# Kernel tuning notes

Measured on AMD Instinct MI355X. Metric: run time of the kernel, lower is better.

The kernel has to match this reference:

```python
import jax, jax.numpy as jnp
import numpy as np

B, N, D, E, H, K = 2, 2048, 1024, 8, 2048, 2


def setup_inputs() -> dict:
    key = jax.random.key(0)
    ks = jax.random.split(key, 5)
    s = 0.02  # init scale
    return {
        "x": jax.random.normal(ks[0], (B, N, D), dtype=jnp.float32),
        "w_gate": jax.random.normal(ks[1], (D, E), dtype=jnp.float32) * s,
        "b_gate": jnp.zeros((E,), dtype=jnp.float32),
        "w1": jax.random.normal(ks[2], (E, D, H), dtype=jnp.float32) * s,
        "b1": jnp.zeros((E, H), dtype=jnp.float32),
        "w2": jax.random.normal(ks[3], (E, H, D), dtype=jnp.float32) * s,
        "b2": jnp.zeros((E, D), dtype=jnp.float32),
    }


def reference(x, w_gate, b_gate, w1, b1, w2, b2):
    b, n, d = x.shape
    T = b * n
    xf = x.reshape(T, d)                                   # (T, D)
    # --- top-k routing ---
    logits = xf @ w_gate + b_gate                          # (T, E)
    topk_logits, topk_idx = jax.lax.top_k(logits, K)       # (T, K)
    topk_gates = jax.nn.softmax(topk_logits, axis=-1)      # softmax over selected experts
    entropy = -(topk_gates * jnp.log(jnp.clip(topk_gates, 1e-8, None))).sum(-1).mean()
    # scatter top-k gates into full (T, E) gate matrix (zeros for unselected)
    gates = jnp.zeros_like(logits).at[jnp.arange(T)[:, None], topk_idx].add(topk_gates)
    # --- expert MLPs (dense over experts; gates zero out unselected) ---
    h = jax.nn.relu(jnp.einsum('td,edh->eth', xf, w1) + b1[:, None, :])  # (E, T, H)
    y = jnp.einsum('eth,ehd->etd', h, w2) + b2[:, None, :]               # (E, T, D)
    out = jnp.einsum('etd,te->td', y, gates).reshape(b, n, d)
    return out, entropy
```

## Files before the change

kernel.cpp:

```cpp
#include <hip/hip_runtime.h>

#define T_TOK 4096
#define D_DIM 1024
#define E_EXP 8
#define H_DIM 2048
#define CAP   9216
#define TILES_M 72

typedef __attribute__((ext_vector_type(8))) short bf16x8;
typedef __attribute__((ext_vector_type(4))) float f32x4;

__device__ inline unsigned short f2bf(float f) {
    unsigned int u = __float_as_uint(f);
    unsigned int r = (u + 0x7fffu + ((u >> 16) & 1u)) >> 16;
    return (unsigned short)r;
}

#define GLD_LDS16(g, l)                                                        \
    __builtin_amdgcn_global_load_lds(                                          \
        (const __attribute__((address_space(1))) void*)(g),                    \
        (__attribute__((address_space(3))) void*)(l), 16, 0, 0)

__global__ __launch_bounds__(256) void tcvt_kernel(const float* __restrict__ src,
                                                   unsigned short* __restrict__ dst,
                                                   int R, int C) {
    __shared__ float tile[64][65];
    size_t eo = (size_t)blockIdx.z * R * C;
    src += eo; dst += eo;
    int tx = threadIdx.x & 15, ty = threadIdx.x >> 4;
    int c0 = blockIdx.x * 64, r0 = blockIdx.y * 64;
    #pragma unroll
    for (int i = 0; i < 4; i++) {
        int row = ty + i * 16;
        float4 v = *(const float4*)&src[(size_t)(r0 + row) * C + c0 + tx * 4];
        tile[row][tx * 4 + 0] = v.x;
        tile[row][tx * 4 + 1] = v.y;
        tile[row][tx * 4 + 2] = v.z;
        tile[row][tx * 4 + 3] = v.w;
    }
    __syncthreads();
    #pragma unroll
    for (int i = 0; i < 4; i++) {
        int cc = ty + i * 16;
        int rr = tx * 4;
        ushort4 o;
        o.x = f2bf(tile[rr + 0][cc]);
        o.y = f2bf(tile[rr + 1][cc]);
        o.z = f2bf(tile[rr + 2][cc]);
        o.w = f2bf(tile[rr + 3][cc]);
        *(ushort4*)&dst[(size_t)(c0 + cc) * R + r0 + rr] = o;
    }
}

__global__ __launch_bounds__(256) void gating_kernel(
    const float* __restrict__ xf, const float* __restrict__ wg,
    const float* __restrict__ bg, unsigned short* __restrict__ xb,
    int* __restrict__ tk_e, float* __restrict__ tk_g,
    float* __restrict__ ent_part)
{
    __shared__ float ents[4];
    int wave = threadIdx.x >> 6, lane = threadIdx.x & 63;
    int t = blockIdx.x * 4 + wave;
    const float* xr = xf + (size_t)t * D_DIM;
    unsigned short* xbr = xb + (size_t)t * D_DIM;
    float acc[8] = {0.f,0.f,0.f,0.f,0.f,0.f,0.f,0.f};
    for (int i = 0; i < 16; i++) {
        int d = lane + i * 64;
        float xv = xr[d];
        xbr[d] = f2bf(xv);
        const float4* wr = (const float4*)(wg + (size_t)d * 8);
        float4 w0 = wr[0], w1 = wr[1];
        acc[0] += xv * w0.x; acc[1] += xv * w0.y; acc[2] += xv * w0.z; acc[3] += xv * w0.w;
        acc[4] += xv * w1.x; acc[5] += xv * w1.y; acc[6] += xv * w1.z; acc[7] += xv * w1.w;
    }
    #pragma unroll
    for (int s = 1; s < 64; s <<= 1) {
        #pragma unroll
        for (int e = 0; e < 8; e++) acc[e] += __shfl_xor(acc[e], s, 64);
    }
    if (lane == 0) {
        float l[8];
        #pragma unroll
        for (int e = 0; e < 8; e++) l[e] = acc[e] + bg[e];
        int i0 = 0;
        #pragma unroll
        for (int e = 1; e < 8; e++) if (l[e] > l[i0]) i0 = e;
        int i1 = (i0 == 0) ? 1 : 0;
        #pragma unroll
        for (int e = 0; e < 8; e++) if (e != i0 && l[e] > l[i1]) i1 = e;
        float z  = expf(l[i1] - l[i0]);
        float p0 = 1.0f / (1.0f + z);
        float p1 = z / (1.0f + z);
        float ent = -(p0 * logf(fmaxf(p0, 1e-8f)) + p1 * logf(fmaxf(p1, 1e-8f)));
        ents[wave] = ent;
        tk_e[t * 2 + 0] = i0; tk_g[t * 2 + 0] = p0;
        tk_e[t * 2 + 1] = i1; tk_g[t * 2 + 1] = p1;
    }
    __syncthreads();
    if (threadIdx.x == 0)
        ent_part[blockIdx.x] = ents[0] + ents[1] + ents[2] + ents[3];
}

__global__ __launch_bounds__(1024) void route_kernel(
    const int* __restrict__ tk_e, const float* __restrict__ tk_g,
    int* __restrict__ off, int* __restrict__ slot_token,
    float* __restrict__ slot_gate, int* __restrict__ slot_of,
    const float* __restrict__ ent_part, float* __restrict__ ent_out)
{
    __shared__ int wt[16][8];
    __shared__ int wx[16][8];
    __shared__ int base[9];
    __shared__ int tot[8];
    __shared__ float es[16];

    int tid = threadIdx.x, wid = tid >> 6, lane = tid & 63;
    int i0 = tid * 8;
    int ev[8];
    *(int4*)&ev[0] = *(const int4*)&tk_e[i0];
    *(int4*)&ev[4] = *(const int4*)&tk_e[i0 + 4];

    float s = ent_part[tid];
    #pragma unroll
    for (int d = 1; d < 64; d <<= 1) s += __shfl_xor(s, d, 64);
    if (lane == 0) es[wid] = s;

    unsigned own[4] = {0u, 0u, 0u, 0u};
    #pragma unroll
    for (int j = 0; j < 8; j++) {
        int e = ev[j];
        int reg = ((e < 4) ? 0 : 2) + (e & 1);
        own[reg] += 1u << (((e >> 1) & 1) * 16);
    }
    unsigned inc[4] = {own[0], own[1], own[2], own[3]};
    #pragma unroll
    for (int d = 1; d < 64; d <<= 1) {
        #pragma unroll
        for (int k = 0; k < 4; k++) {
            unsigned t = __shfl_up(inc[k], d, 64);
            if (lane >= d) inc[k] += t;
        }
    }
    if (lane == 63) {
        #pragma unroll
        for (int e = 0; e < 8; e++) {
            int reg = ((e < 4) ? 0 : 2) + (e & 1);
            wt[wid][e] = (inc[reg] >> (((e >> 1) & 1) * 16)) & 0xFFFF;
        }
    }
    __syncthreads();
    if (tid == 0) {
        int o = 0;
        for (int e = 0; e < 8; e++) {
            int run = 0;
            for (int w = 0; w < 16; w++) { wx[w][e] = run; run += wt[w][e]; }
            tot[e] = run;
            base[e] = o;
            off[e] = o;
            o += (run + 127) & ~127;
        }
        base[8] = o;
        off[8] = o;
        float se = 0.f;
        for (int w = 0; w < 16; w++) se += es[w];
        *ent_out = se * (1.0f / T_TOK);
    }
    __syncthreads();

    #pragma unroll
    for (int e = 0; e < 8; e++) {
        int p0 = base[e] + tot[e], p1 = base[e + 1];
        for (int i = p0 + tid; i < p1; i += 1024) slot_token[i] = -1;
    }

    unsigned run[4] = {0u, 0u, 0u, 0u};
    #pragma unroll
    for (int j = 0; j < 8; j++) {
        int e = ev[j];
        int reg = ((e < 4) ? 0 : 2) + (e & 1);
        int sh = ((e >> 1) & 1) * 16;
        int lx = (int)(((inc[reg] - own[reg]) >> sh) & 0xFFFF);
        int lr = (int)((run[reg] >> sh) & 0xFFFF);
        int slot = base[e] + wx[wid][e] + lx + lr;
        run[reg] += 1u << sh;
        int i = i0 + j;
        slot_token[slot] = i >> 1;
        slot_gate[slot] = tk_g[i];
        slot_of[i] = slot;
    }
}

__global__ __launch_bounds__(256) void gemm1_kernel(
    const unsigned short* __restrict__ xb, const unsigned short* __restrict__ w1t,
    const float* __restrict__ b1g, const int* __restrict__ off,
    const int* __restrict__ slot_token, unsigned short* __restrict__ Hb)
{
    __shared__ __align__(16) unsigned short As[128 * 32];
    __shared__ __align__(16) unsigned short Bs[128 * 32];

    int s0 = blockIdx.x * 128;
    if (s0 >= off[E_EXP]) return;
    int e = 0;
    while (s0 >= off[e + 1]) e++;
    int n0 = blockIdx.y * 128;

    int tid = threadIdx.x;
    int wave = tid >> 6, lane = tid & 63;
    int lrow = lane & 15, quad = lane >> 4;
    int srow = lane >> 2;
    int scol = ((lane & 3) ^ ((srow >> 1) & 3)) * 8;

    int r0 = 16 * wave + srow, r1 = r0 + 64;
    int t0 = slot_token[s0 + r0]; if (t0 < 0) t0 = 0;
    int t1 = slot_token[s0 + r1]; if (t1 < 0) t1 = 0;
    const unsigned short* wb = w1t + (size_t)e * H_DIM * D_DIM;
    const unsigned short* a0 = xb + (size_t)t0 * D_DIM + scol;
    const unsigned short* a1 = xb + (size_t)t1 * D_DIM + scol;
    const unsigned short* bp0 = wb + (size_t)(n0 + r0) * D_DIM + scol;
    const unsigned short* bp1 = wb + (size_t)(n0 + r1) * D_DIM + scol;

    unsigned short* lA0 = As + (16 * wave) * 32;
    unsigned short* lA1 = As + (64 + 16 * wave) * 32;
    unsigned short* lB0 = Bs + (16 * wave) * 32;
    unsigned short* lB1 = Bs + (64 + 16 * wave) * 32;

    f32x4 acc[4][4];
    #pragma unroll
    for (int mi = 0; mi < 4; mi++)
        #pragma unroll
        for (int ni = 0; ni < 4; ni++) acc[mi][ni] = (f32x4){0.f, 0.f, 0.f, 0.f};

    int wr = (wave >> 1) * 64, wc = (wave & 1) * 64;
    int g = (quad ^ ((lrow >> 1) & 3)) * 8;

    for (int k0 = 0; k0 < D_DIM; k0 += 32) {
        __syncthreads();
        GLD_LDS16(a0 + k0, lA0);
        GLD_LDS16(a1 + k0, lA1);
        GLD_LDS16(bp0 + k0, lB0);
        GLD_LDS16(bp1 + k0, lB1);
        __syncthreads();
        bf16x8 af[4], bfr[4];
        #pragma unroll
        for (int i = 0; i < 4; i++) {
            af[i]  = *(const bf16x8*)&As[(wr + i * 16 + lrow) * 32 + g];
            bfr[i] = *(const bf16x8*)&Bs[(wc + i * 16 + lrow) * 32 + g];
        }
        #pragma unroll
        for (int mi = 0; mi < 4; mi++)
            #pragma unroll
            for (int ni = 0; ni < 4; ni++)
                acc[mi][ni] = __builtin_amdgcn_mfma_f32_16x16x32_bf16(
                    af[mi], bfr[ni], acc[mi][ni], 0, 0, 0);
    }

    float bv[4];
    #pragma unroll
    for (int ni = 0; ni < 4; ni++) bv[ni] = b1g[e * H_DIM + n0 + wc + ni * 16 + lrow];
    unsigned short* w = As + wave * 1024;
    __syncthreads();
    #pragma unroll
    for (int mi = 0; mi < 4; mi++) {
        #pragma unroll
        for (int ni = 0; ni < 4; ni++)
            #pragma unroll
            for (int r = 0; r < 4; r++)
                w[(quad * 4 + r) * 64 + ni * 16 + lrow] =
                    f2bf(fmaxf(acc[mi][ni][r] + bv[ni], 0.0f));
        int rd = lane >> 3, cc = (lane & 7) * 8;
        bf16x8 v0 = *(const bf16x8*)&w[rd * 64 + cc];
        bf16x8 v1 = *(const bf16x8*)&w[(8 + rd) * 64 + cc];
        size_t rowg = (size_t)(s0 + wr + mi * 16 + rd) * H_DIM + n0 + wc + cc;
        *(bf16x8*)&Hb[rowg] = v0;
        *(bf16x8*)&Hb[rowg + 8 * H_DIM] = v1;
    }
}

__global__ __launch_bounds__(256) void gemm2_kernel(
    const unsigned short* __restrict__ Hb, const unsigned short* __restrict__ w2t,
    const float* __restrict__ b2g, const int* __restrict__ off,
    unsigned short* __restrict__ Yb)
{
    __shared__ __align__(16) unsigned short As[128 * 32];
    __shared__ __align__(16) unsigned short Bs[128 * 32];

    int s0 = blockIdx.x * 128;
    if (s0 >= off[E_EXP]) return;
    int e = 0;
    while (s0 >= off[e + 1]) e++;
    int n0 = blockIdx.y * 128;

    int tid = threadIdx.x;
    int wave = tid >> 6, lane = tid & 63;
    int lrow = lane & 15, quad = lane >> 4;
    int srow = lane >> 2;
    int scol = ((lane & 3) ^ ((srow >> 1) & 3)) * 8;

    int r0 = 16 * wave + srow, r1 = r0 + 64;
    const unsigned short* wb = w2t + (size_t)e * D_DIM * H_DIM;
    const unsigned short* a0 = Hb + (size_t)(s0 + r0) * H_DIM + scol;
    const unsigned short* a1 = Hb + (size_t)(s0 + r1) * H_DIM + scol;
    const unsigned short* bp0 = wb + (size_t)(n0 + r0) * H_DIM + scol;
    const unsigned short* bp1 = wb + (size_t)(n0 + r1) * H_DIM + scol;

    unsigned short* lA0 = As + (16 * wave) * 32;
    unsigned short* lA1 = As + (64 + 16 * wave) * 32;
    unsigned short* lB0 = Bs + (16 * wave) * 32;
    unsigned short* lB1 = Bs + (64 + 16 * wave) * 32;

    f32x4 acc[4][4];
    #pragma unroll
    for (int mi = 0; mi < 4; mi++)
        #pragma unroll
        for (int ni = 0; ni < 4; ni++) acc[mi][ni] = (f32x4){0.f, 0.f, 0.f, 0.f};

    int wr = (wave >> 1) * 64, wc = (wave & 1) * 64;
    int g = (quad ^ ((lrow >> 1) & 3)) * 8;

    for (int k0 = 0; k0 < H_DIM; k0 += 32) {
        __syncthreads();
        GLD_LDS16(a0 + k0, lA0);
        GLD_LDS16(a1 + k0, lA1);
        GLD_LDS16(bp0 + k0, lB0);
        GLD_LDS16(bp1 + k0, lB1);
        __syncthreads();
        bf16x8 af[4], bfr[4];
        #pragma unroll
        for (int i = 0; i < 4; i++) {
            af[i]  = *(const bf16x8*)&As[(wr + i * 16 + lrow) * 32 + g];
            bfr[i] = *(const bf16x8*)&Bs[(wc + i * 16 + lrow) * 32 + g];
        }
        #pragma unroll
        for (int mi = 0; mi < 4; mi++)
            #pragma unroll
            for (int ni = 0; ni < 4; ni++)
                acc[mi][ni] = __builtin_amdgcn_mfma_f32_16x16x32_bf16(
                    af[mi], bfr[ni], acc[mi][ni], 0, 0, 0);
    }

    float bv[4];
    #pragma unroll
    for (int ni = 0; ni < 4; ni++) bv[ni] = b2g[e * D_DIM + n0 + wc + ni * 16 + lrow];
    unsigned short* w = As + wave * 1024;
    __syncthreads();
    #pragma unroll
    for (int mi = 0; mi < 4; mi++) {
        #pragma unroll
        for (int ni = 0; ni < 4; ni++)
            #pragma unroll
            for (int r = 0; r < 4; r++)
                w[(quad * 4 + r) * 64 + ni * 16 + lrow] = f2bf(acc[mi][ni][r] + bv[ni]);
        int rd = lane >> 3, cc = (lane & 7) * 8;
        bf16x8 v0 = *(const bf16x8*)&w[rd * 64 + cc];
        bf16x8 v1 = *(const bf16x8*)&w[(8 + rd) * 64 + cc];
        size_t rowg = (size_t)(s0 + wr + mi * 16 + rd) * D_DIM + n0 + wc + cc;
        *(bf16x8*)&Yb[rowg] = v0;
        *(bf16x8*)&Yb[rowg + 8 * D_DIM] = v1;
    }
}

__global__ __launch_bounds__(256) void combine_kernel(
    const unsigned short* __restrict__ Yb, const int* __restrict__ slot_of,
    const float* __restrict__ tk_g, float* __restrict__ out)
{
    int t = blockIdx.x * 2 + (threadIdx.x >> 7);
    int j = threadIdx.x & 127;
    int sA = slot_of[t * 2], sB = slot_of[t * 2 + 1];
    float gA = tk_g[t * 2], gB = tk_g[t * 2 + 1];
    uint4 va = *(const uint4*)(Yb + (size_t)sA * D_DIM + j * 8);
    uint4 vb = *(const uint4*)(Yb + (size_t)sB * D_DIM + j * 8);
    const unsigned int* pa = (const unsigned int*)&va;
    const unsigned int* pb = (const unsigned int*)&vb;
    float o[8];
    #pragma unroll
    for (int i = 0; i < 4; i++) {
        float a_lo = __uint_as_float(pa[i] << 16);
        float a_hi = __uint_as_float(pa[i] & 0xffff0000u);
        float b_lo = __uint_as_float(pb[i] << 16);
        float b_hi = __uint_as_float(pb[i] & 0xffff0000u);
        o[i * 2 + 0] = gA * a_lo + gB * b_lo;
        o[i * 2 + 1] = gA * a_hi + gB * b_hi;
    }
    float* op = out + (size_t)t * D_DIM + j * 8;
    ((float4*)op)[0] = make_float4(o[0], o[1], o[2], o[3]);
    ((float4*)op)[1] = make_float4(o[4], o[5], o[6], o[7]);
}

extern "C" void kernel_launch(void* const* d_in, const int* in_sizes, int n_in,
                              void* d_out, int out_size, void* d_ws, size_t ws_size,
                              hipStream_t stream)
{
    const float* xf = (const float*)d_in[0];
    const float* wg = (const float*)d_in[1];
    const float* bg = (const float*)d_in[2];
    const float* w1 = (const float*)d_in[3];
    const float* b1 = (const float*)d_in[4];
    const float* w2 = (const float*)d_in[5];
    const float* b2 = (const float*)d_in[6];
    float* out = (float*)d_out;

    char* p = (char*)d_ws;
    int* off    = (int*)p;
    int* tk_e   = off + 16;
    float* tk_g = (float*)(tk_e + T_TOK * 2);
    int* slot_token = (int*)(tk_g + T_TOK * 2);
    float* slot_gate = (float*)(slot_token + CAP);
    int* slot_of = (int*)(slot_gate + CAP);
    float* ent_part = (float*)(slot_of + T_TOK * 2);
    size_t ofs = ((size_t)((char*)(ent_part + T_TOK / 4) - p) + 255) & ~(size_t)255;
    unsigned short* xb  = (unsigned short*)(p + ofs); ofs += (size_t)T_TOK * D_DIM * 2;
    unsigned short* w1t = (unsigned short*)(p + ofs); ofs += (size_t)E_EXP * D_DIM * H_DIM * 2;
    unsigned short* w2t = (unsigned short*)(p + ofs); ofs += (size_t)E_EXP * H_DIM * D_DIM * 2;
    unsigned short* Hb  = (unsigned short*)(p + ofs); ofs += (size_t)CAP * H_DIM * 2;
    unsigned short* Yb  = w1t;

    gating_kernel<<<T_TOK / 4, 256, 0, stream>>>(xf, wg, bg, xb, tk_e, tk_g, ent_part);
    route_kernel<<<1, 1024, 0, stream>>>(tk_e, tk_g, off, slot_token, slot_gate, slot_of,
                                         ent_part, out + (size_t)T_TOK * D_DIM);
    tcvt_kernel<<<dim3(H_DIM / 64, D_DIM / 64, E_EXP), 256, 0, stream>>>(w1, w1t, D_DIM, H_DIM);
    tcvt_kernel<<<dim3(D_DIM / 64, H_DIM / 64, E_EXP), 256, 0, stream>>>(w2, w2t, H_DIM, D_DIM);
    gemm1_kernel<<<dim3(TILES_M, H_DIM / 128), 256, 0, stream>>>(xb, w1t, b1, off,
                                                                 slot_token, Hb);
    gemm2_kernel<<<dim3(TILES_M, D_DIM / 128), 256, 0, stream>>>(Hb, w2t, b2, off, Yb);
    combine_kernel<<<T_TOK / 2, 256, 0, stream>>>(Yb, slot_of, tk_g, out);
}
```

Before: 330.0 us.

## Merge expert GEMMs into templated 8-wave kernel with 4-stage LDS pipeline

Replaces the two separate expert GEMM kernels with one templated kernel that uses 512 threads, 256-row M tiles and a four-buffer LDS ring filled by direct global-to-LDS loads, with manual vmcnt waits and barriers so loads overlap MFMA work. Expert segments are padded to 256 rows and capacity grows to match, so the M grid shrinks. The aim is to hide global memory latency and double the reuse of each weight tile per block. The cost is more padded rows of wasted compute, higher LDS use per block, and fragile hand-written wait counts.

```diff
diff --git a/kernel.cpp b/kernel.cpp
--- a/kernel.cpp
+++ b/kernel.cpp
@@ -4,8 +4,8 @@
 #define D_DIM 1024
 #define E_EXP 8
 #define H_DIM 2048
-#define CAP   9216
-#define TILES_M 72
+#define CAP   10240
+#define TILES_M 40
 
 typedef __attribute__((ext_vector_type(8))) short bf16x8;
 typedef __attribute__((ext_vector_type(4))) float f32x4;
@@ -156,7 +156,7 @@
             tot[e] = run;
             base[e] = o;
             off[e] = o;
-            o += (run + 127) & ~127;
+            o += (run + 255) & ~255;
         }
         base[8] = o;
         off[8] = o;
@@ -189,39 +189,49 @@
     }
 }
 
-__global__ __launch_bounds__(256) void gemm1_kernel(
-    const unsigned short* __restrict__ xb, const unsigned short* __restrict__ w1t,
-    const float* __restrict__ b1g, const int* __restrict__ off,
-    const int* __restrict__ slot_token, unsigned short* __restrict__ Hb)
-{
-    __shared__ __align__(16) unsigned short As[128 * 32];
-    __shared__ __align__(16) unsigned short Bs[128 * 32];
-
-    int s0 = blockIdx.x * 128;
+template<int KD, int ND, bool GATHER, bool RELU>
+__global__ __launch_bounds__(512, 2) void gemm8p_kernel(
+    const unsigned short* __restrict__ Ag, const unsigned short* __restrict__ Bw,
+    const float* __restrict__ bias, const int* __restrict__ off,
+    const int* __restrict__ slot_token, unsigned short* __restrict__ Out)
+{
+    constexpr int NT = KD / 32;
+    __shared__ __align__(16) unsigned short smem[49152];
+
+    int s0 = blockIdx.x * 256;
     if (s0 >= off[E_EXP]) return;
     int e = 0;
     while (s0 >= off[e + 1]) e++;
     int n0 = blockIdx.y * 128;
 
     int tid = threadIdx.x;
-    int wave = tid >> 6, lane = tid & 63;
-    int lrow = lane & 15, quad = lane >> 4;
-    int srow = lane >> 2;
-    int scol = ((lane & 3) ^ ((srow >> 1) & 3)) * 8;
-
-    int r0 = 16 * wave + srow, r1 = r0 + 64;
-    int t0 = slot_token[s0 + r0]; if (t0 < 0) t0 = 0;
-    int t1 = slot_token[s0 + r1]; if (t1 < 0) t1 = 0;
-    const unsigned short* wb = w1t + (size_t)e * H_DIM * D_DIM;
-    const unsigned short* a0 = xb + (size_t)t0 * D_DIM + scol;
-    const unsigned short* a1 = xb + (size_t)t1 * D_DIM + scol;
-    const unsigned short* bp0 = wb + (size_t)(n0 + r0) * D_DIM + scol;
-    const unsigned short* bp1 = wb + (size_t)(n0 + r1) * D_DIM + scol;
-
-    unsigned short* lA0 = As + (16 * wave) * 32;
-    unsigned short* lA1 = As + (64 + 16 * wave) * 32;
-    unsigned short* lB0 = Bs + (16 * wave) * 32;
-    unsigned short* lB1 = Bs + (64 + 16 * wave) * 32;
+    int w = tid >> 6, lane = tid & 63;
+    int wm = w >> 1, wn = w & 1;
+    int lrow = lane & 15, q = lane >> 4;
+    int lr = lane >> 2;
+    int clg = ((lane & 3) ^ ((lane >> 3) & 3)) * 8;
+
+    int rA0 = w * 32 + lr, rA1 = rA0 + 16;
+    int rB  = w * 16 + lr;
+
+    const unsigned short* aS0;
+    const unsigned short* aS1;
+    if constexpr (GATHER) {
+        int t0 = slot_token[s0 + rA0]; if (t0 < 0) t0 = 0;
+        int t1 = slot_token[s0 + rA1]; if (t1 < 0) t1 = 0;
+        aS0 = Ag + (size_t)t0 * KD + clg;
+        aS1 = Ag + (size_t)t1 * KD + clg;
+    } else {
+        aS0 = Ag + (size_t)(s0 + rA0) * KD + clg;
+        aS1 = Ag + (size_t)(s0 + rA1) * KD + clg;
+    }
+    const unsigned short* bS = Bw + (size_t)e * ND * KD + (size_t)(n0 + rB) * KD + clg;
+
+    int stA = w * 1024;
+    int stB = 8192 + w * 512;
+    int swz = (q ^ ((lrow >> 1) & 3)) << 3;
+    int aoff = (wm * 64 + lrow) * 32 + swz;
+    int boff = 8192 + (wn * 64 + lrow) * 32 + swz;
 
     f32x4 acc[4][4];
     #pragma unroll
@@ -229,132 +239,76 @@
         #pragma unroll
         for (int ni = 0; ni < 4; ni++) acc[mi][ni] = (f32x4){0.f, 0.f, 0.f, 0.f};
 
-    int wr = (wave >> 1) * 64, wc = (wave & 1) * 64;
-    int g = (quad ^ ((lrow >> 1) & 3)) * 8;
-
-    for (int k0 = 0; k0 < D_DIM; k0 += 32) {
-        __syncthreads();
-        GLD_LDS16(a0 + k0, lA0);
-        GLD_LDS16(a1 + k0, lA1);
-        GLD_LDS16(bp0 + k0, lB0);
-        GLD_LDS16(bp1 + k0, lB1);
-        __syncthreads();
-        bf16x8 af[4], bfr[4];
-        #pragma unroll
-        for (int i = 0; i < 4; i++) {
-            af[i]  = *(const bf16x8*)&As[(wr + i * 16 + lrow) * 32 + g];
-            bfr[i] = *(const bf16x8*)&Bs[(wc + i * 16 + lrow) * 32 + g];
-        }
-        #pragma unroll
-        for (int mi = 0; mi < 4; mi++)
-            #pragma unroll
-            for (int ni = 0; ni < 4; ni++)
-                acc[mi][ni] = __builtin_amdgcn_mfma_f32_16x16x32_bf16(
-                    af[mi], bfr[ni], acc[mi][ni], 0, 0, 0);
-    }
+    #pragma unroll
+    for (int u = 0; u < 3; u++) {
+        GLD_LDS16(aS0 + u * 32, smem + u * 12288 + stA);
+        GLD_LDS16(aS1 + u * 32, smem + u * 12288 + stA + 512);
+        GLD_LDS16(bS  + u * 32, smem + u * 12288 + stB);
+    }
+    asm volatile("s_waitcnt vmcnt(6)" ::: "memory");
+    asm volatile("s_barrier" ::: "memory");
+
+#define PHASE(RP, RS, U, DOST, VM)                                             \
+    {                                                                          \
+        bf16x8 af[4], bfr[4];                                                  \
+        _Pragma("unroll")                                                      \
+        for (int i = 0; i < 4; i++) {                                          \
+            af[i]  = *(const bf16x8*)&smem[(RP) * 12288 + aoff + i * 512];     \
+            bfr[i] = *(const bf16x8*)&smem[(RP) * 12288 + boff + i * 512];     \
+        }                                                                      \
+        if (DOST) {                                                            \
+            GLD_LDS16(aS0 + (size_t)(U) * 32, smem + (RS) * 12288 + stA);      \
+            GLD_LDS16(aS1 + (size_t)(U) * 32, smem + (RS) * 12288 + stA + 512);\
+            GLD_LDS16(bS  + (size_t)(U) * 32, smem + (RS) * 12288 + stB);      \
+        }                                                                      \
+        asm volatile("s_barrier" ::: "memory");                                \
+        asm volatile("s_waitcnt lgkmcnt(0)" ::: "memory");                     \
+        __builtin_amdgcn_s_setprio(1);                                         \
+        _Pragma("unroll")                                                      \
+        for (int mi = 0; mi < 4; mi++)                                         \
+            _Pragma("unroll")                                                  \
+            for (int ni = 0; ni < 4; ni++)                                     \
+                acc[mi][ni] = __builtin_amdgcn_mfma_f32_16x16x32_bf16(         \
+                    af[mi], bfr[ni], acc[mi][ni], 0, 0, 0);                    \
+        __builtin_amdgcn_s_setprio(0);                                         \
+        asm volatile("s_waitcnt vmcnt(" VM ")" ::: "memory");                  \
+        asm volatile("s_barrier" ::: "memory");                                \
+    }
+
+    int t4 = 0;
+    for (; t4 + 8 <= NT; t4 += 4) {
+        PHASE(0, 3, t4 + 3, true, "6")
+        PHASE(1, 0, t4 + 4, true, "6")
+        PHASE(2, 1, t4 + 5, true, "6")
+        PHASE(3, 2, t4 + 6, true, "6")
+    }
+    PHASE(0, 3, t4 + 3, true,  "6")
+    PHASE(1, 0, 0,      false, "3")
+    PHASE(2, 1, 0,      false, "0")
+    PHASE(3, 2, 0,      false, "63")
+#undef PHASE
 
     float bv[4];
     #pragma unroll
-    for (int ni = 0; ni < 4; ni++) bv[ni] = b1g[e * H_DIM + n0 + wc + ni * 16 + lrow];
-    unsigned short* w = As + wave * 1024;
-    __syncthreads();
+    for (int ni = 0; ni < 4; ni++)
+        bv[ni] = bias[(size_t)e * ND + n0 + wn * 64 + ni * 16 + lrow];
+    unsigned short* scr = smem + w * 1024;
     #pragma unroll
     for (int mi = 0; mi < 4; mi++) {
         #pragma unroll
         for (int ni = 0; ni < 4; ni++)
             #pragma unroll
-            for (int r = 0; r < 4; r++)
-                w[(quad * 4 + r) * 64 + ni * 16 + lrow] =
-                    f2bf(fmaxf(acc[mi][ni][r] + bv[ni], 0.0f));
+            for (int r = 0; r < 4; r++) {
+                float v = acc[mi][ni][r] + bv[ni];
+                if constexpr (RELU) v = fmaxf(v, 0.0f);
+                scr[(q * 4 + r) * 64 + ni * 16 + lrow] = f2bf(v);
+            }
         int rd = lane >> 3, cc = (lane & 7) * 8;
-        bf16x8 v0 = *(const bf16x8*)&w[rd * 64 + cc];
-        bf16x8 v1 = *(const bf16x8*)&w[(8 + rd) * 64 + cc];
-        size_t rowg = (size_t)(s0 + wr + mi * 16 + rd) * H_DIM + n0 + wc + cc;
-        *(bf16x8*)&Hb[rowg] = v0;
-        *(bf16x8*)&Hb[rowg + 8 * H_DIM] = v1;
-    }
-}
-
-__global__ __launch_bounds__(256) void gemm2_kernel(
-    const unsigned short* __restrict__ Hb, const unsigned short* __restrict__ w2t,
-    const float* __restrict__ b2g, const int* __restrict__ off,
-    unsigned short* __restrict__ Yb)
-{
-    __shared__ __align__(16) unsigned short As[128 * 32];
-    __shared__ __align__(16) unsigned short Bs[128 * 32];
-
-    int s0 = blockIdx.x * 128;
-    if (s0 >= off[E_EXP]) return;
-    int e = 0;
-    while (s0 >= off[e + 1]) e++;
-    int n0 = blockIdx.y * 128;
-
-    int tid = threadIdx.x;
-    int wave = tid >> 6, lane = tid & 63;
-    int lrow = lane & 15, quad = lane >> 4;
-    int srow = lane >> 2;
-    int scol = ((lane & 3) ^ ((srow >> 1) & 3)) * 8;
-
-    int r0 = 16 * wave + srow, r1 = r0 + 64;
-    const unsigned short* wb = w2t + (size_t)e * D_DIM * H_DIM;
-    const unsigned short* a0 = Hb + (size_t)(s0 + r0) * H_DIM + scol;
-    const unsigned short* a1 = Hb + (size_t)(s0 + r1) * H_DIM + scol;
-    const unsigned short* bp0 = wb + (size_t)(n0 + r0) * H_DIM + scol;
-    const unsigned short* bp1 = wb + (size_t)(n0 + r1) * H_DIM + scol;
-
-    unsigned short* lA0 = As + (16 * wave) * 32;
-    unsigned short* lA1 = As + (64 + 16 * wave) * 32;
-    unsigned short* lB0 = Bs + (16 * wave) * 32;
-    unsigned short* lB1 = Bs + (64 + 16 * wave) * 32;
-
-    f32x4 acc[4][4];
-    #pragma unroll
-    for (int mi = 0; mi < 4; mi++)
-        #pragma unroll
-        for (int ni = 0; ni < 4; ni++) acc[mi][ni] = (f32x4){0.f, 0.f, 0.f, 0.f};
-
-    int wr = (wave >> 1) * 64, wc = (wave & 1) * 64;
-    int g = (quad ^ ((lrow >> 1) & 3)) * 8;
-
-    for (int k0 = 0; k0 < H_DIM; k0 += 32) {
-        __syncthreads();
-        GLD_LDS16(a0 + k0, lA0);
-        GLD_LDS16(a1 + k0, lA1);
-        GLD_LDS16(bp0 + k0, lB0);
-        GLD_LDS16(bp1 + k0, lB1);
-        __syncthreads();
-        bf16x8 af[4], bfr[4];
-        #pragma unroll
-        for (int i = 0; i < 4; i++) {
-            af[i]  = *(const bf16x8*)&As[(wr + i * 16 + lrow) * 32 + g];
-            bfr[i] = *(const bf16x8*)&Bs[(wc + i * 16 + lrow) * 32 + g];
-        }
-        #pragma unroll
-        for (int mi = 0; mi < 4; mi++)
-            #pragma unroll
-            for (int ni = 0; ni < 4; ni++)
-                acc[mi][ni] = __builtin_amdgcn_mfma_f32_16x16x32_bf16(
-                    af[mi], bfr[ni], acc[mi][ni], 0, 0, 0);
-    }
-
-    float bv[4];
-    #pragma unroll
-    for (int ni = 0; ni < 4; ni++) bv[ni] = b2g[e * D_DIM + n0 + wc + ni * 16 + lrow];
-    unsigned short* w = As + wave * 1024;
-    __syncthreads();
-    #pragma unroll
-    for (int mi = 0; mi < 4; mi++) {
-        #pragma unroll
-        for (int ni = 0; ni < 4; ni++)
-            #pragma unroll
-            for (int r = 0; r < 4; r++)
-                w[(quad * 4 + r) * 64 + ni * 16 + lrow] = f2bf(acc[mi][ni][r] + bv[ni]);
-        int rd = lane >> 3, cc = (lane & 7) * 8;
-        bf16x8 v0 = *(const bf16x8*)&w[rd * 64 + cc];
-        bf16x8 v1 = *(const bf16x8*)&w[(8 + rd) * 64 + cc];
-        size_t rowg = (size_t)(s0 + wr + mi * 16 + rd) * D_DIM + n0 + wc + cc;
-        *(bf16x8*)&Yb[rowg] = v0;
-        *(bf16x8*)&Yb[rowg + 8 * D_DIM] = v1;
+        bf16x8 v0 = *(const bf16x8*)&scr[rd * 64 + cc];
+        bf16x8 v1 = *(const bf16x8*)&scr[(8 + rd) * 64 + cc];
+        size_t rowg = (size_t)(s0 + wm * 64 + mi * 16 + rd) * ND + n0 + wn * 64 + cc;
+        *(bf16x8*)&Out[rowg] = v0;
+        *(bf16x8*)&Out[rowg + 8 * (size_t)ND] = v1;
     }
 }
 
@@ -418,8 +372,9 @@
                                          ent_part, out + (size_t)T_TOK * D_DIM);
     tcvt_kernel<<<dim3(H_DIM / 64, D_DIM / 64, E_EXP), 256, 0, stream>>>(w1, w1t, D_DIM, H_DIM);
     tcvt_kernel<<<dim3(D_DIM / 64, H_DIM / 64, E_EXP), 256, 0, stream>>>(w2, w2t, H_DIM, D_DIM);
-    gemm1_kernel<<<dim3(TILES_M, H_DIM / 128), 256, 0, stream>>>(xb, w1t, b1, off,
-                                                                 slot_token, Hb);
-    gemm2_kernel<<<dim3(TILES_M, D_DIM / 128), 256, 0, stream>>>(Hb, w2t, b2, off, Yb);
+    gemm8p_kernel<D_DIM, H_DIM, true, true>
+        <<<dim3(TILES_M, H_DIM / 128), 512, 0, stream>>>(xb, w1t, b1, off, slot_token, Hb);
+    gemm8p_kernel<H_DIM, D_DIM, false, false>
+        <<<dim3(TILES_M, D_DIM / 128), 512, 0, stream>>>(Hb, w2t, b2, off, slot_token, Yb);
     combine_kernel<<<T_TOK / 2, 256, 0, stream>>>(Yb, slot_of, tk_g, out);
 }
```

Result: no change. 326.9 us (-0.9%).

## Double-buffer LDS tiles in expert GEMMs and remap workgroups across XCDs

Applied to the files above, without the earlier changes.

Merges the two expert GEMM kernels into one template, with flags for token gather and ReLU. The template double-buffers the A and B LDS tiles so the next k-step's global-to-LDS loads are issued before the current step's MFMAs, leaving one barrier per iteration instead of two. It also remaps workgroup IDs so consecutive tiles land on the same XCD, aiming for better L2 reuse of shared weight and activation tiles. The cost is twice the LDS per block, which may reduce occupancy. Correctness depends on the async LDS loads having completed before the barrier.

```diff
diff --git a/kernel.cpp b/kernel.cpp
--- a/kernel.cpp
+++ b/kernel.cpp
@@ -189,19 +189,28 @@
     }
 }
 
-__global__ __launch_bounds__(256) void gemm1_kernel(
-    const unsigned short* __restrict__ xb, const unsigned short* __restrict__ w1t,
-    const float* __restrict__ b1g, const int* __restrict__ off,
-    const int* __restrict__ slot_token, unsigned short* __restrict__ Hb)
-{
-    __shared__ __align__(16) unsigned short As[128 * 32];
-    __shared__ __align__(16) unsigned short Bs[128 * 32];
-
-    int s0 = blockIdx.x * 128;
+template<int KD, int ND, bool GATHER, bool RELU>
+__global__ __launch_bounds__(256) void gemm2p_kernel(
+    const unsigned short* __restrict__ Ag, const unsigned short* __restrict__ Bw,
+    const float* __restrict__ bias, const int* __restrict__ off,
+    const int* __restrict__ slot_token, unsigned short* __restrict__ Out)
+{
+    __shared__ __align__(16) unsigned short As[2][128 * 32];
+    __shared__ __align__(16) unsigned short Bs[2][128 * 32];
+
+    int nwgx = gridDim.x;
+    int nwg = nwgx * gridDim.y;
+    int orig = blockIdx.y * nwgx + blockIdx.x;
+    int q = nwg >> 3, r = nwg & 7;
+    int xcd = orig & 7, idx = orig >> 3;
+    int nid = (xcd < r ? xcd * (q + 1) : r * (q + 1) + (xcd - r) * q) + idx;
+    int bx = nid % nwgx, by = nid / nwgx;
+
+    int s0 = bx * 128;
     if (s0 >= off[E_EXP]) return;
     int e = 0;
     while (s0 >= off[e + 1]) e++;
-    int n0 = blockIdx.y * 128;
+    int n0 = by * 128;
 
     int tid = threadIdx.x;
     int wave = tid >> 6, lane = tid & 63;
@@ -210,18 +219,23 @@
     int scol = ((lane & 3) ^ ((srow >> 1) & 3)) * 8;
 
     int r0 = 16 * wave + srow, r1 = r0 + 64;
-    int t0 = slot_token[s0 + r0]; if (t0 < 0) t0 = 0;
-    int t1 = slot_token[s0 + r1]; if (t1 < 0) t1 = 0;
-    const unsigned short* wb = w1t + (size_t)e * H_DIM * D_DIM;
-    const unsigned short* a0 = xb + (size_t)t0 * D_DIM + scol;
-    const unsigned short* a1 = xb + (size_t)t1 * D_DIM + scol;
-    const unsigned short* bp0 = wb + (size_t)(n0 + r0) * D_DIM + scol;
-    const unsigned short* bp1 = wb + (size_t)(n0 + r1) * D_DIM + scol;
-
-    unsigned short* lA0 = As + (16 * wave) * 32;
-    unsigned short* lA1 = As + (64 + 16 * wave) * 32;
-    unsigned short* lB0 = Bs + (16 * wave) * 32;
-    unsigned short* lB1 = Bs + (64 + 16 * wave) * 32;
+    const unsigned short* a0;
+    const unsigned short* a1;
+    if constexpr (GATHER) {
+        int t0 = slot_token[s0 + r0]; if (t0 < 0) t0 = 0;
+        int t1 = slot_token[s0 + r1]; if (t1 < 0) t1 = 0;
+        a0 = Ag + (size_t)t0 * KD + scol;
+        a1 = Ag + (size_t)t1 * KD + scol;
+    } else {
+        a0 = Ag + (size_t)(s0 + r0) * KD + scol;
+        a1 = Ag + (size_t)(s0 + r1) * KD + scol;
+    }
+    const unsigned short* wb = Bw + (size_t)e * ND * KD;
+    const unsigned short* bp0 = wb + (size_t)(n0 + r0) * KD + scol;
+    const unsigned short* bp1 = wb + (size_t)(n0 + r1) * KD + scol;
+
+    int stA0 = (16 * wave) * 32;
+    int stA1 = (64 + 16 * wave) * 32;
 
     f32x4 acc[4][4];
     #pragma unroll
@@ -232,18 +246,26 @@
     int wr = (wave >> 1) * 64, wc = (wave & 1) * 64;
     int g = (quad ^ ((lrow >> 1) & 3)) * 8;
 
-    for (int k0 = 0; k0 < D_DIM; k0 += 32) {
-        __syncthreads();
-        GLD_LDS16(a0 + k0, lA0);
-        GLD_LDS16(a1 + k0, lA1);
-        GLD_LDS16(bp0 + k0, lB0);
-        GLD_LDS16(bp1 + k0, lB1);
-        __syncthreads();
+    GLD_LDS16(a0,  &As[0][stA0]);
+    GLD_LDS16(a1,  &As[0][stA1]);
+    GLD_LDS16(bp0, &Bs[0][stA0]);
+    GLD_LDS16(bp1, &Bs[0][stA1]);
+    __syncthreads();
+
+    constexpr int NT = KD / 32;
+    int cur = 0;
+    for (int t = 0; t < NT - 1; ++t) {
+        int nb = cur ^ 1;
+        int k1 = (t + 1) * 32;
+        GLD_LDS16(a0 + k1,  &As[nb][stA0]);
+        GLD_LDS16(a1 + k1,  &As[nb][stA1]);
+        GLD_LDS16(bp0 + k1, &Bs[nb][stA0]);
+        GLD_LDS16(bp1 + k1, &Bs[nb][stA1]);
         bf16x8 af[4], bfr[4];
         #pragma unroll
         for (int i = 0; i < 4; i++) {
-            af[i]  = *(const bf16x8*)&As[(wr + i * 16 + lrow) * 32 + g];
-            bfr[i] = *(const bf16x8*)&Bs[(wc + i * 16 + lrow) * 32 + g];
+            af[i]  = *(const bf16x8*)&As[cur][(wr + i * 16 + lrow) * 32 + g];
+            bfr[i] = *(const bf16x8*)&Bs[cur][(wc + i * 16 + lrow) * 32 + g];
         }
         #pragma unroll
         for (int mi = 0; mi < 4; mi++)
@@ -251,83 +273,15 @@
             for (int ni = 0; ni < 4; ni++)
                 acc[mi][ni] = __builtin_amdgcn_mfma_f32_16x16x32_bf16(
                     af[mi], bfr[ni], acc[mi][ni], 0, 0, 0);
-    }
-
-    float bv[4];
-    #pragma unroll
-    for (int ni = 0; ni < 4; ni++) bv[ni] = b1g[e * H_DIM + n0 + wc + ni * 16 + lrow];
-    unsigned short* w = As + wave * 1024;
-    __syncthreads();
-    #pragma unroll
-    for (int mi = 0; mi < 4; mi++) {
-        #pragma unroll
-        for (int ni = 0; ni < 4; ni++)
-            #pragma unroll
-            for (int r = 0; r < 4; r++)
-                w[(quad * 4 + r) * 64 + ni * 16 + lrow] =
-                    f2bf(fmaxf(acc[mi][ni][r] + bv[ni], 0.0f));
-        int rd = lane >> 3, cc = (lane & 7) * 8;
-        bf16x8 v0 = *(const bf16x8*)&w[rd * 64 + cc];
-        bf16x8 v1 = *(const bf16x8*)&w[(8 + rd) * 64 + cc];
-        size_t rowg = (size_t)(s0 + wr + mi * 16 + rd) * H_DIM + n0 + wc + cc;
-        *(bf16x8*)&Hb[rowg] = v0;
-        *(bf16x8*)&Hb[rowg + 8 * H_DIM] = v1;
-    }
-}
-
-__global__ __launch_bounds__(256) void gemm2_kernel(
-    const unsigned short* __restrict__ Hb, const unsigned short* __restrict__ w2t,
-    const float* __restrict__ b2g, const int* __restrict__ off,
-    unsigned short* __restrict__ Yb)
-{
-    __shared__ __align__(16) unsigned short As[128 * 32];
-    __shared__ __align__(16) unsigned short Bs[128 * 32];
-
-    int s0 = blockIdx.x * 128;
-    if (s0 >= off[E_EXP]) return;
-    int e = 0;
-    while (s0 >= off[e + 1]) e++;
-    int n0 = blockIdx.y * 128;
-
-    int tid = threadIdx.x;
-    int wave = tid >> 6, lane = tid & 63;
-    int lrow = lane & 15, quad = lane >> 4;
-    int srow = lane >> 2;
-    int scol = ((lane & 3) ^ ((srow >> 1) & 3)) * 8;
-
-    int r0 = 16 * wave + srow, r1 = r0 + 64;
-    const unsigned short* wb = w2t + (size_t)e * D_DIM * H_DIM;
-    const unsigned short* a0 = Hb + (size_t)(s0 + r0) * H_DIM + scol;
-    const unsigned short* a1 = Hb + (size_t)(s0 + r1) * H_DIM + scol;
-    const unsigned short* bp0 = wb + (size_t)(n0 + r0) * H_DIM + scol;
-    const unsigned short* bp1 = wb + (size_t)(n0 + r1) * H_DIM + scol;
-
-    unsigned short* lA0 = As + (16 * wave) * 32;
-    unsigned short* lA1 = As + (64 + 16 * wave) * 32;
-    unsigned short* lB0 = Bs + (16 * wave) * 32;
-    unsigned short* lB1 = Bs + (64 + 16 * wave) * 32;
-
-    f32x4 acc[4][4];
-    #pragma unroll
-    for (int mi = 0; mi < 4; mi++)
-        #pragma unroll
-        for (int ni = 0; ni < 4; ni++) acc[mi][ni] = (f32x4){0.f, 0.f, 0.f, 0.f};
-
-    int wr = (wave >> 1) * 64, wc = (wave & 1) * 64;
-    int g = (quad ^ ((lrow >> 1) & 3)) * 8;
-
-    for (int k0 = 0; k0 < H_DIM; k0 += 32) {
         __syncthreads();
-        GLD_LDS16(a0 + k0, lA0);
-        GLD_LDS16(a1 + k0, lA1);
-        GLD_LDS16(bp0 + k0, lB0);
-        GLD_LDS16(bp1 + k0, lB1);
-        __syncthreads();
+        cur = nb;
+    }
+    {
         bf16x8 af[4], bfr[4];
         #pragma unroll
         for (int i = 0; i < 4; i++) {
-            af[i]  = *(const bf16x8*)&As[(wr + i * 16 + lrow) * 32 + g];
-            bfr[i] = *(const bf16x8*)&Bs[(wc + i * 16 + lrow) * 32 + g];
+            af[i]  = *(const bf16x8*)&As[cur][(wr + i * 16 + lrow) * 32 + g];
+            bfr[i] = *(const bf16x8*)&Bs[cur][(wc + i * 16 + lrow) * 32 + g];
         }
         #pragma unroll
         for (int mi = 0; mi < 4; mi++)
@@ -339,22 +293,26 @@
 
     float bv[4];
     #pragma unroll
-    for (int ni = 0; ni < 4; ni++) bv[ni] = b2g[e * D_DIM + n0 + wc + ni * 16 + lrow];
-    unsigned short* w = As + wave * 1024;
+    for (int ni = 0; ni < 4; ni++)
+        bv[ni] = bias[(size_t)e * ND + n0 + wc + ni * 16 + lrow];
+    unsigned short* w = &As[0][0] + wave * 1024;
     __syncthreads();
     #pragma unroll
     for (int mi = 0; mi < 4; mi++) {
         #pragma unroll
         for (int ni = 0; ni < 4; ni++)
             #pragma unroll
-            for (int r = 0; r < 4; r++)
-                w[(quad * 4 + r) * 64 + ni * 16 + lrow] = f2bf(acc[mi][ni][r] + bv[ni]);
+            for (int rr = 0; rr < 4; rr++) {
+                float v = acc[mi][ni][rr] + bv[ni];
+                if constexpr (RELU) v = fmaxf(v, 0.0f);
+                w[(quad * 4 + rr) * 64 + ni * 16 + lrow] = f2bf(v);
+            }
         int rd = lane >> 3, cc = (lane & 7) * 8;
         bf16x8 v0 = *(const bf16x8*)&w[rd * 64 + cc];
         bf16x8 v1 = *(const bf16x8*)&w[(8 + rd) * 64 + cc];
-        size_t rowg = (size_t)(s0 + wr + mi * 16 + rd) * D_DIM + n0 + wc + cc;
-        *(bf16x8*)&Yb[rowg] = v0;
-        *(bf16x8*)&Yb[rowg + 8 * D_DIM] = v1;
+        size_t rowg = (size_t)(s0 + wr + mi * 16 + rd) * ND + n0 + wc + cc;
+        *(bf16x8*)&Out[rowg] = v0;
+        *(bf16x8*)&Out[rowg + 8 * (size_t)ND] = v1;
     }
 }
 
@@ -418,8 +376,9 @@
                                          ent_part, out + (size_t)T_TOK * D_DIM);
     tcvt_kernel<<<dim3(H_DIM / 64, D_DIM / 64, E_EXP), 256, 0, stream>>>(w1, w1t, D_DIM, H_DIM);
     tcvt_kernel<<<dim3(D_DIM / 64, H_DIM / 64, E_EXP), 256, 0, stream>>>(w2, w2t, H_DIM, D_DIM);
-    gemm1_kernel<<<dim3(TILES_M, H_DIM / 128), 256, 0, stream>>>(xb, w1t, b1, off,
-                                                                 slot_token, Hb);
-    gemm2_kernel<<<dim3(TILES_M, D_DIM / 128), 256, 0, stream>>>(Hb, w2t, b2, off, Yb);
+    gemm2p_kernel<D_DIM, H_DIM, true, true>
+        <<<dim3(TILES_M, H_DIM / 128), 256, 0, stream>>>(xb, w1t, b1, off, slot_token, Hb);
+    gemm2p_kernel<H_DIM, D_DIM, false, false>
+        <<<dim3(TILES_M, D_DIM / 128), 256, 0, stream>>>(Hb, w2t, b2, off, slot_token, Yb);
     combine_kernel<<<T_TOK / 2, 256, 0, stream>>>(Yb, slot_of, tk_g, out);
 }
```

New measurement: 371.1 us. +12.5%, slower.
